# Kernel tuning notes

Measured on AMD Instinct MI355X. Metric: run time of the kernel, lower is better.

Reference implementation:

```python
import jax, jax.numpy as jnp
import numpy as np

N_SAMPLES = 8_000_000
NB_CLASSES = 5


def setup_inputs() -> dict:
    key = jax.random.key(0)
    k1, k2 = jax.random.split(key)
    preds = jax.random.normal(k1, (N_SAMPLES, NB_CLASSES), dtype=jnp.float32)
    true = jax.random.randint(k2, (N_SAMPLES,), 0, NB_CLASSES, dtype=jnp.int32)
    return {"preds": preds, "true": true}


def reference(preds, true):
    N, C = preds.shape
    dt = preds.dtype
    cls = jnp.arange(C, dtype=dt)

    # SoftArgmax1D per row (base_index=0, step_size=1), then round -> hard class
    soft_arg = jax.nn.softmax(preds, axis=1) @ cls            # [N]
    pred_idx = jnp.clip(jnp.round(soft_arg).astype(jnp.int32), 0, C - 1)

    # confusion_matrix[true, pred] += 1 via fused scatter-add on flat index
    flat = true * C + pred_idx                                 # [N]
    conf = jnp.zeros((C * C,), dtype=dt).at[flat].add(1.0).reshape(C, C)

    # quadratic kappa weights: (i-j)^2 / (C-1)^2
    weights = (cls[:, None] - cls[None, :]) ** 2 / ((C - 1) ** 2)

    # class histograms (scatter-add)
    true_hist = jnp.zeros((C,), dtype=dt).at[true].add(1.0)
    pred_hist = jnp.zeros((C,), dtype=dt).at[pred_idx].add(1.0)

    # expected matrix E = outer(true_hist, pred_hist), both normalized
    E = jnp.outer(true_hist, pred_hist)
    E = E / E.sum()
    conf = conf / conf.sum()

    num = (conf * weights).sum()
    den = (E * weights).sum()
    return num / den
```

## Files before the change

### kernel.cpp

```cpp
#include <hip/hip_runtime.h>
#include <math.h>

#define NCLS 5
#define NBINS 25
#define NTHREADS 256
#define NBLOCKS 768
#define ROWS_PER_CHUNK 256
#define CHUNK_PRED_F4 320
#define PRED_SEGS 5

__device__ __forceinline__ void gload_lds16(const void* g, void* l) {
    __builtin_amdgcn_global_load_lds(
        (const __attribute__((address_space(1))) unsigned int*)(const unsigned int*)g,
        (__attribute__((address_space(3))) unsigned int*)(unsigned int*)l,
        16, 0, 0);
}

__global__ void __launch_bounds__(NTHREADS)
kappa_count(const float* __restrict__ preds,
            const int* __restrict__ truev,
            int N,
            unsigned int* __restrict__ partials) {
    __shared__ float s_pred[2][4][ROWS_PER_CHUNK * NCLS];
    __shared__ int   s_lab [2][4][ROWS_PER_CHUNK];
    __shared__ unsigned int s_conf[4 * 32];

    const int tid = threadIdx.x;
    const int wv = tid >> 6;
    const int lane = tid & 63;
    if (tid < 128) s_conf[tid] = 0u;
    __syncthreads();
    unsigned int* hist = &s_conf[wv << 5];

    const int nchunks = N / ROWS_PER_CHUNK;
    const int wgid = blockIdx.x * 4 + wv;
    const int wstride = gridDim.x * 4;

    auto stage = [&](int c, int b) {
        const float4* sp = (const float4*)preds + (size_t)c * CHUNK_PRED_F4;
        #pragma unroll
        for (int k = 0; k < PRED_SEGS; ++k)
            gload_lds16(sp + k * 64 + lane,
                        &s_pred[b][wv][k * 256]);
        const int4* sl = (const int4*)(truev + (size_t)c * ROWS_PER_CHUNK);
        gload_lds16(sl + lane, &s_lab[b][wv][0]);
    };

    auto dorow = [&](float r0, float r1, float r2, float r3, float r4, int t) {
        float m = fmaxf(fmaxf(fmaxf(fmaxf(r0, r1), r2), r3), r4);
        float e0 = __expf(r0 - m), e1 = __expf(r1 - m), e2 = __expf(r2 - m),
              e3 = __expf(r3 - m), e4 = __expf(r4 - m);
        float s = e0 + e1 + e2 + e3 + e4;
        float dot = e1 + e2 * 2.f + e3 * 3.f + e4 * 4.f;
        int pi = (int)rintf(dot / s);
        pi = min(max(pi, 0), NCLS - 1);
        atomicAdd(&hist[t * NCLS + pi], 1u);
    };

    int c = wgid, cur = 0;
    if (c < nchunks) stage(c, 0);
    for (; c < nchunks; c += wstride) {
        const int cn = c + wstride;
        if (cn < nchunks) {
            stage(cn, cur ^ 1);
            asm volatile("s_waitcnt vmcnt(6)" ::: "memory");
        } else {
            asm volatile("s_waitcnt vmcnt(0)" ::: "memory");
        }
        const float* bp = s_pred[cur][wv];
        const int* lp = s_lab[cur][wv];
        #pragma unroll
        for (int rr = 0; rr < 4; ++rr) {
            const int r = lane + (rr << 6);
            const float* rp = bp + r * NCLS;
            dorow(rp[0], rp[1], rp[2], rp[3], rp[4], lp[r]);
        }
        cur ^= 1;
    }

    if (blockIdx.x == 0 && wv == 0) {
        for (int r = nchunks * ROWS_PER_CHUNK + lane; r < N; r += 64) {
            float v0 = preds[(size_t)r * NCLS + 0];
            float v1 = preds[(size_t)r * NCLS + 1];
            float v2 = preds[(size_t)r * NCLS + 2];
            float v3 = preds[(size_t)r * NCLS + 3];
            float v4 = preds[(size_t)r * NCLS + 4];
            dorow(v0, v1, v2, v3, v4, truev[r]);
        }
    }

    __syncthreads();
    if (tid < NBINS)
        partials[(size_t)tid * gridDim.x + blockIdx.x] =
            s_conf[tid] + s_conf[32 + tid] + s_conf[64 + tid] + s_conf[96 + tid];
}

__global__ void kappa_final(const unsigned int* __restrict__ partials,
                            int nb,
                            float* __restrict__ out) {
    __shared__ double s_bin[NBINS];
    const int tid = threadIdx.x;
    const int bin = tid >> 5;
    const int l = tid & 31;

    if (bin < NBINS) {
        unsigned int acc = 0u;
        const unsigned int* p = partials + (size_t)bin * nb;
        for (int j = l; j < nb; j += 32) acc += p[j];
        #pragma unroll
        for (int off = 16; off > 0; off >>= 1)
            acc += __shfl_down(acc, off, 32);
        if (l == 0) s_bin[bin] = (double)acc;
    }
    __syncthreads();

    if (tid == 0) {
        double tot = 0.0;
        for (int i = 0; i < NBINS; i++) tot += s_bin[i];
        double th[NCLS] = {0, 0, 0, 0, 0};
        double ph[NCLS] = {0, 0, 0, 0, 0};
        for (int i = 0; i < NCLS; i++)
            for (int j = 0; j < NCLS; j++) {
                th[i] += s_bin[i * NCLS + j];
                ph[j] += s_bin[i * NCLS + j];
            }
        double num = 0.0, den = 0.0;
        for (int i = 0; i < NCLS; i++)
            for (int j = 0; j < NCLS; j++) {
                double w = (double)((i - j) * (i - j)) / 16.0;
                num += w * s_bin[i * NCLS + j];
                den += w * th[i] * ph[j];
            }
        out[0] = (float)(num * tot / den);
    }
}

extern "C" void kernel_launch(void* const* d_in, const int* in_sizes, int n_in,
                              void* d_out, int out_size, void* d_ws, size_t ws_size,
                              hipStream_t stream) {
    const float* preds = (const float*)d_in[0];
    const int* truev = (const int*)d_in[1];
    const int N = in_sizes[1];

    int nblocks = NBLOCKS;
    size_t need = (size_t)nblocks * NBINS * sizeof(unsigned int);
    if (need > ws_size) nblocks = (int)(ws_size / (NBINS * sizeof(unsigned int)));
    unsigned int* partials = (unsigned int*)d_ws;

    kappa_count<<<nblocks, NTHREADS, 0, stream>>>(preds, truev, N, partials);
    kappa_final<<<1, 1024, 0, stream>>>(partials, nblocks, (float*)d_out);
}
```

Measured before the change: 246.5 us.

## Deepen LDS staging pipeline to four buffers with smaller per-wave chunks

Replaces double-buffered 256-row chunks with a four-stage ring of 128-row chunks per wave, issuing three chunks ahead via global_load_lds. Explicit vmcnt waits are tuned for the four loads per stage, with a drain loop that counts the remaining in-flight chunks. The intent is to keep more memory requests in flight to hide HBM latency in this bandwidth-bound pass. The risks are more loop overhead per row, half-idle lanes on the partial loads, and fragile hand-written vmcnt counts.

```diff
diff --git a/kernel.cpp b/kernel.cpp
--- a/kernel.cpp
+++ b/kernel.cpp
@@ -5,9 +5,10 @@
 #define NBINS 25
 #define NTHREADS 256
 #define NBLOCKS 768
-#define ROWS_PER_CHUNK 256
-#define CHUNK_PRED_F4 320
-#define PRED_SEGS 5
+#define ROWS 128
+#define DEPTH 4
+#define CHUNK_F4 160
+#define LPC 4
 
 __device__ __forceinline__ void gload_lds16(const void* g, void* l) {
     __builtin_amdgcn_global_load_lds(
@@ -21,8 +22,8 @@
             const int* __restrict__ truev,
             int N,
             unsigned int* __restrict__ partials) {
-    __shared__ float s_pred[2][4][ROWS_PER_CHUNK * NCLS];
-    __shared__ int   s_lab [2][4][ROWS_PER_CHUNK];
+    __shared__ float s_pred[DEPTH][4][ROWS * NCLS];
+    __shared__ int   s_lab [DEPTH][4][ROWS];
     __shared__ unsigned int s_conf[4 * 32];
 
     const int tid = threadIdx.x;
@@ -32,18 +33,19 @@
     __syncthreads();
     unsigned int* hist = &s_conf[wv << 5];
 
-    const int nchunks = N / ROWS_PER_CHUNK;
+    const int nchunks = N / ROWS;
     const int wgid = blockIdx.x * 4 + wv;
     const int wstride = gridDim.x * 4;
 
     auto stage = [&](int c, int b) {
-        const float4* sp = (const float4*)preds + (size_t)c * CHUNK_PRED_F4;
-        #pragma unroll
-        for (int k = 0; k < PRED_SEGS; ++k)
-            gload_lds16(sp + k * 64 + lane,
-                        &s_pred[b][wv][k * 256]);
-        const int4* sl = (const int4*)(truev + (size_t)c * ROWS_PER_CHUNK);
-        gload_lds16(sl + lane, &s_lab[b][wv][0]);
+        const float4* sp = (const float4*)preds + (size_t)c * CHUNK_F4;
+        gload_lds16(sp + lane,       &s_pred[b][wv][0]);
+        gload_lds16(sp + 64 + lane,  &s_pred[b][wv][256]);
+        if (lane < 32) {
+            gload_lds16(sp + 128 + lane, &s_pred[b][wv][512]);
+            gload_lds16((const int4*)truev + (size_t)c * 32 + lane,
+                        &s_lab[b][wv][0]);
+        }
     };
 
     auto dorow = [&](float r0, float r1, float r2, float r3, float r4, int t) {
@@ -57,29 +59,45 @@
         atomicAdd(&hist[t * NCLS + pi], 1u);
     };
 
-    int c = wgid, cur = 0;
-    if (c < nchunks) stage(c, 0);
-    for (; c < nchunks; c += wstride) {
-        const int cn = c + wstride;
-        if (cn < nchunks) {
-            stage(cn, cur ^ 1);
-            asm volatile("s_waitcnt vmcnt(6)" ::: "memory");
-        } else {
-            asm volatile("s_waitcnt vmcnt(0)" ::: "memory");
-        }
-        const float* bp = s_pred[cur][wv];
-        const int* lp = s_lab[cur][wv];
+    auto compute = [&](int b) {
+        const float* bp = s_pred[b][wv];
+        const int* lp = s_lab[b][wv];
         #pragma unroll
-        for (int rr = 0; rr < 4; ++rr) {
+        for (int rr = 0; rr < 2; ++rr) {
             const int r = lane + (rr << 6);
             const float* rp = bp + r * NCLS;
             dorow(rp[0], rp[1], rp[2], rp[3], rp[4], lp[r]);
         }
-        cur ^= 1;
+    };
+
+    int c = wgid;
+    int cb = 0;
+    #pragma unroll
+    for (int k = 0; k < DEPTH - 1; ++k) {
+        const int ck = c + k * wstride;
+        if (ck < nchunks) stage(ck, k);
+    }
+
+    for (; c + (DEPTH - 1) * wstride < nchunks; c += wstride) {
+        stage(c + (DEPTH - 1) * wstride, (cb + DEPTH - 1) & 3);
+        asm volatile("s_waitcnt vmcnt(12)" ::: "memory");
+        compute(cb);
+        cb = (cb + 1) & 3;
+    }
+
+    int rem = 0;
+    for (int cc = c; cc < nchunks; cc += wstride) rem++;
+    for (; c < nchunks; c += wstride) {
+        rem--;
+        if (rem >= 2)      asm volatile("s_waitcnt vmcnt(8)" ::: "memory");
+        else if (rem == 1) asm volatile("s_waitcnt vmcnt(4)" ::: "memory");
+        else               asm volatile("s_waitcnt vmcnt(0)" ::: "memory");
+        compute(cb);
+        cb = (cb + 1) & 3;
     }
 
     if (blockIdx.x == 0 && wv == 0) {
-        for (int r = nchunks * ROWS_PER_CHUNK + lane; r < N; r += 64) {
+        for (int r = nchunks * ROWS + lane; r < N; r += 64) {
             float v0 = preds[(size_t)r * NCLS + 0];
             float v1 = preds[(size_t)r * NCLS + 1];
             float v2 = preds[(size_t)r * NCLS + 2];
```

Measured after the change: 248.2 us. Within noise of the previous version (+0.7%).

## Replace direct global-to-LDS loads with register double-buffered prefetch

Applied to the files above, without the earlier changes.

Drops the global_load_lds async staging with its double-buffered LDS arrays and manual vmcnt waits. Each wave now prefetches two chunks ahead into registers (two sets of float4 and label arrays), writes the current chunk to a single LDS buffer and reads it back transposed per row. Labels come straight from registers instead of LDS. The grid grows from 768 to 1024 blocks with an occupancy hint of 4. This cuts LDS footprint and uses plain vector loads, at the cost of more registers and an extra LDS write per chunk.

```diff
diff --git a/kernel.cpp b/kernel.cpp
--- a/kernel.cpp
+++ b/kernel.cpp
@@ -4,25 +4,16 @@
 #define NCLS 5
 #define NBINS 25
 #define NTHREADS 256
-#define NBLOCKS 768
-#define ROWS_PER_CHUNK 256
-#define CHUNK_PRED_F4 320
-#define PRED_SEGS 5
+#define NBLOCKS 1024
+#define ROWS 256
+#define CHUNK_F4 320
 
-__device__ __forceinline__ void gload_lds16(const void* g, void* l) {
-    __builtin_amdgcn_global_load_lds(
-        (const __attribute__((address_space(1))) unsigned int*)(const unsigned int*)g,
-        (__attribute__((address_space(3))) unsigned int*)(unsigned int*)l,
-        16, 0, 0);
-}
-
-__global__ void __launch_bounds__(NTHREADS)
+__global__ void __launch_bounds__(NTHREADS, 4)
 kappa_count(const float* __restrict__ preds,
             const int* __restrict__ truev,
             int N,
             unsigned int* __restrict__ partials) {
-    __shared__ float s_pred[2][4][ROWS_PER_CHUNK * NCLS];
-    __shared__ int   s_lab [2][4][ROWS_PER_CHUNK];
+    __shared__ float s_pred[4][ROWS * NCLS];
     __shared__ unsigned int s_conf[4 * 32];
 
     const int tid = threadIdx.x;
@@ -32,18 +23,23 @@
     __syncthreads();
     unsigned int* hist = &s_conf[wv << 5];
 
-    const int nchunks = N / ROWS_PER_CHUNK;
+    const int nchunks = N / ROWS;
     const int wgid = blockIdx.x * 4 + wv;
-    const int wstride = gridDim.x * 4;
+    const int ws = gridDim.x * 4;
 
-    auto stage = [&](int c, int b) {
-        const float4* sp = (const float4*)preds + (size_t)c * CHUNK_PRED_F4;
+    auto loadset = [&](int c, float4 (&pa)[5], int (&lb)[4]) {
+        const float4* sp = (const float4*)preds + (size_t)c * CHUNK_F4 + lane;
         #pragma unroll
-        for (int k = 0; k < PRED_SEGS; ++k)
-            gload_lds16(sp + k * 64 + lane,
-                        &s_pred[b][wv][k * 256]);
-        const int4* sl = (const int4*)(truev + (size_t)c * ROWS_PER_CHUNK);
-        gload_lds16(sl + lane, &s_lab[b][wv][0]);
+        for (int s = 0; s < 5; ++s) pa[s] = sp[s * 64];
+        const int* tb = truev + (size_t)c * ROWS + lane;
+        #pragma unroll
+        for (int r = 0; r < 4; ++r) lb[r] = tb[r * 64];
+    };
+
+    auto writeset = [&](const float4 (&pa)[5]) {
+        float4* dst = (float4*)&s_pred[wv][0];
+        #pragma unroll
+        for (int s = 0; s < 5; ++s) dst[s * 64 + lane] = pa[s];
     };
 
     auto dorow = [&](float r0, float r1, float r2, float r3, float r4, int t) {
@@ -57,29 +53,44 @@
         atomicAdd(&hist[t * NCLS + pi], 1u);
     };
 
-    int c = wgid, cur = 0;
-    if (c < nchunks) stage(c, 0);
-    for (; c < nchunks; c += wstride) {
-        const int cn = c + wstride;
-        if (cn < nchunks) {
-            stage(cn, cur ^ 1);
-            asm volatile("s_waitcnt vmcnt(6)" ::: "memory");
-        } else {
-            asm volatile("s_waitcnt vmcnt(0)" ::: "memory");
+    auto computechunk = [&](int l0, int l1, int l2, int l3) {
+        const float* bp = s_pred[wv];
+        const float* rp0 = bp + lane * NCLS;
+        const float* rp1 = bp + (lane + 64) * NCLS;
+        const float* rp2 = bp + (lane + 128) * NCLS;
+        const float* rp3 = bp + (lane + 192) * NCLS;
+        dorow(rp0[0], rp0[1], rp0[2], rp0[3], rp0[4], l0);
+        dorow(rp1[0], rp1[1], rp1[2], rp1[3], rp1[4], l1);
+        dorow(rp2[0], rp2[1], rp2[2], rp2[3], rp2[4], l2);
+        dorow(rp3[0], rp3[1], rp3[2], rp3[3], rp3[4], l3);
+    };
+
+    float4 pA[5], pB[5];
+    int lA[4], lB[4];
+    int c = wgid;
+    if (c < nchunks) loadset(c, pA, lA);
+    if (c + ws < nchunks) loadset(c + ws, pB, lB);
+
+    while (c < nchunks) {
+        {
+            int l0 = lA[0], l1 = lA[1], l2 = lA[2], l3 = lA[3];
+            writeset(pA);
+            if (c + 2 * ws < nchunks) loadset(c + 2 * ws, pA, lA);
+            computechunk(l0, l1, l2, l3);
         }
-        const float* bp = s_pred[cur][wv];
-        const int* lp = s_lab[cur][wv];
-        #pragma unroll
-        for (int rr = 0; rr < 4; ++rr) {
-            const int r = lane + (rr << 6);
-            const float* rp = bp + r * NCLS;
-            dorow(rp[0], rp[1], rp[2], rp[3], rp[4], lp[r]);
+        c += ws;
+        if (c >= nchunks) break;
+        {
+            int l0 = lB[0], l1 = lB[1], l2 = lB[2], l3 = lB[3];
+            writeset(pB);
+            if (c + 2 * ws < nchunks) loadset(c + 2 * ws, pB, lB);
+            computechunk(l0, l1, l2, l3);
         }
-        cur ^= 1;
+        c += ws;
     }
 
     if (blockIdx.x == 0 && wv == 0) {
-        for (int r = nchunks * ROWS_PER_CHUNK + lane; r < N; r += 64) {
+        for (int r = nchunks * ROWS + lane; r < N; r += 64) {
             float v0 = preds[(size_t)r * NCLS + 0];
             float v1 = preds[(size_t)r * NCLS + 1];
             float v2 = preds[(size_t)r * NCLS + 2];
```

After: 269.2 us. +9.2%, slower.
